# Performance work log

Measured on AMD Instinct MI355X. Metric: run time of the kernel, lower is better.

Reference implementation:

```python
import jax, jax.numpy as jnp
from jax import lax
import numpy as np

B, T, D = 16, 4096, 512          # batch, encoder length, d_model
C, FW = 10, 100                  # aconv_chans, aconv_filts (kernel width 2*FW+1)
SHARP = 2.0                      # sharpening_factor


def setup_inputs() -> dict:
    key = jax.random.key(0)
    ks = jax.random.split(key, 11)
    s = 1.0 / np.sqrt(D)
    sc = 1.0 / np.sqrt(2 * FW + 1)
    return {
        "value": jax.random.normal(ks[0], (B, T, D), jnp.float32),
        "query": jax.random.normal(ks[1], (B, D), jnp.float32),
        "input_lengths": jax.random.randint(ks[2], (B,), T // 2, T + 1),
        "att_prev": jax.random.uniform(ks[3], (B, T), jnp.float32),
        # learned parameters (torch Linear stores W as [out,in]; y = x @ W.T + b)
        "W_enc": jax.random.uniform(ks[4], (D, D), jnp.float32, -s, s),
        "b_enc": jax.random.uniform(ks[5], (D,), jnp.float32, -s, s),
        "W_dec": jax.random.uniform(ks[6], (D, D), jnp.float32, -s, s),
        "W_att": jax.random.uniform(ks[7], (D, C), jnp.float32, -s, s),
        "W_conv": jax.random.uniform(ks[8], (C, 1, 2 * FW + 1), jnp.float32, -sc, sc),
        "w_g": jax.random.uniform(ks[9], (1, D), jnp.float32, -s, s),
        "b_g": jax.random.uniform(ks[10], (1,), jnp.float32, -s, s),
    }


def reference(value, query, input_lengths, att_prev,
              W_enc, b_enc, W_dec, W_att, W_conv, w_g, b_g):
    # pre_compute_enc_h = mlp_enc(enc_h): [B,T,D]
    pre_enc = jnp.einsum('btd,ed->bte', value, W_enc) + b_enc
    # dec_z_tiled = mlp_dec(dec_z): [B,1,D]
    dec_tiled = (query @ W_dec.T)[:, None, :]
    # loc_conv: 1D conv over T, in_ch=1 -> out_ch=C, same padding -> [B,C,T]
    conv = lax.conv_general_dilated(att_prev[:, None, :], W_conv,
                                    window_strides=(1,), padding=[(FW, FW)],
                                    dimension_numbers=('NCH', 'OIH', 'NCH'))
    # mlp_att on transposed conv: [B,T,C] @ W_att.T -> [B,T,D]
    att_conv = jnp.einsum('bct,dc->btd', conv, W_att)
    # e = gvec(tanh(sum)): [B,T]
    e = jnp.einsum('btd,d->bt', jnp.tanh(att_conv + pre_enc + dec_tiled), w_g[0]) + b_g[0]
    # pad mask: positions >= length are masked to -inf (use large finite neg)
    pad_mask = jnp.arange(T)[None, :] >= input_lengths[:, None]
    e = jnp.where(pad_mask, -1e30, e)
    att_weights = jax.nn.softmax(SHARP * e, axis=1)            # [B,T]
    context = jnp.einsum('btd,bt->bd', value, att_weights)     # [B,D]
    return context, att_weights
```

## Files before the change

kernel.cpp:

```cpp
#include <hip/hip_runtime.h>
#include <hip/hip_bf16.h>

constexpr int kB  = 16;
constexpr int kT  = 4096;
constexpr int kD  = 512;
constexpr int kC  = 10;
constexpr int kFW = 100;
constexpr int kKW = 2 * kFW + 1;
constexpr int kKP = 544;
constexpr int kCW = 32;

typedef __attribute__((ext_vector_type(8))) short short8_t;
typedef __attribute__((ext_vector_type(4))) float float4_t;

__device__ __forceinline__ float tanh_fast(float x) {
  float ax = fabsf(x);
  float z  = __expf(-2.0f * ax);
  float r  = (1.0f - z) / (1.0f + z);
  return copysignf(r, x);
}

__device__ __forceinline__ short f2bf(float x) {
  unsigned u = __float_as_uint(x);
  u += 0x7fffu + ((u >> 16) & 1u);
  return (short)(u >> 16);
}

__device__ __forceinline__ unsigned pk2(float lo, float hi) {
  __hip_bfloat162 h = __float22bfloat162_rn(make_float2(lo, hi));
  union { __hip_bfloat162 h2; unsigned u; } cv; cv.h2 = h; return cv.u;
}

__device__ __forceinline__ void glds16(const void* g, void* l) {
  __builtin_amdgcn_global_load_lds(
      (const __attribute__((address_space(1))) void*)g,
      (__attribute__((address_space(3))) void*)l, 16, 0, 0);
}

__global__ void dec_bias_kernel(const float* __restrict__ query,
                                const float* __restrict__ W_dec,
                                const float* __restrict__ b_enc,
                                float* __restrict__ bias) {
  int gw   = (blockIdx.x * blockDim.x + threadIdx.x) >> 6;
  int lane = threadIdx.x & 63;
  int b = gw >> 9;
  int d = gw & (kD - 1);
  const float* q = query + (size_t)b * kD;
  const float* w = W_dec + (size_t)d * kD;
  float s = 0.f;
#pragma unroll
  for (int k0 = 0; k0 < kD; k0 += 256) {
    float4 qa = *(const float4*)(q + k0 + lane * 4);
    float4 wa = *(const float4*)(w + k0 + lane * 4);
    s += qa.x * wa.x + qa.y * wa.y + qa.z * wa.z + qa.w * wa.w;
  }
#pragma unroll
  for (int off = 32; off > 0; off >>= 1) s += __shfl_down(s, off, 64);
  if (lane == 0) bias[gw] = b_enc[d] + s;
}

__global__ void pack_w_kernel(const float* __restrict__ W_enc,
                              const float* __restrict__ W_att,
                              short* __restrict__ Wbf) {
  int d = blockIdx.x;
  for (int c = threadIdx.x; c < kKP; c += 256) {
    float v = 0.f;
    if (c < kD)            v = W_enc[(size_t)d * kD + c];
    else if (c < kD + kC)  v = W_att[(size_t)d * kC + (c - kD)];
    Wbf[(size_t)d * kKP + c] = f2bf(v);
  }
}

__global__ void conv_kernel(const float* __restrict__ att_prev,
                            const float* __restrict__ W_conv,
                            short* __restrict__ convbf) {
  __shared__ float ap[256 + 2 * kFW];
  __shared__ float wc[kC * kKW];
  int b   = blockIdx.y;
  int t0  = blockIdx.x * 256;
  int tid = threadIdx.x;
  for (int i = tid; i < kC * kKW; i += 256) wc[i] = W_conv[i];
  for (int i = tid; i < 256 + 2 * kFW; i += 256) {
    int p = t0 - kFW + i;
    ap[i] = (p >= 0 && p < kT) ? att_prev[(size_t)b * kT + p] : 0.f;
  }
  __syncthreads();
  float acc[kC];
#pragma unroll
  for (int c = 0; c < kC; ++c) acc[c] = 0.f;
  for (int j = 0; j < kKW; ++j) {
    float a = ap[tid + j];
#pragma unroll
    for (int c = 0; c < kC; ++c) acc[c] += a * wc[c * kKW + j];
  }
  unsigned ow[16];
#pragma unroll
  for (int i = 0; i < 5; ++i) ow[i] = pk2(acc[2 * i], acc[2 * i + 1]);
#pragma unroll
  for (int i = 5; i < 16; ++i) ow[i] = 0u;
  uint4* out = (uint4*)(convbf + ((size_t)b * kT + t0 + tid) * kCW);
  out[0] = make_uint4(ow[0], ow[1], ow[2], ow[3]);
  out[1] = make_uint4(ow[4], ow[5], ow[6], ow[7]);
  out[2] = make_uint4(ow[8], ow[9], ow[10], ow[11]);
  out[3] = make_uint4(ow[12], ow[13], ow[14], ow[15]);
}

constexpr int BM = 128, BN = 128, BK = 32;

__global__ __launch_bounds__(256) void e_kernel(
    const float* __restrict__ value, const short* __restrict__ convbf,
    const short* __restrict__ Wbf, const float* __restrict__ bias,
    const float* __restrict__ w_g, const int* __restrict__ lens,
    float* __restrict__ e_part) {
  __shared__ short As[BM * BK];
  __shared__ short Bs[BN * BK];

  int tid = threadIdx.x;
  int L    = blockIdx.x;
  int xcd  = L & 7;
  int slot = L >> 3;
  int bn   = slot & 3;
  int mt   = xcd * 64 + (slot >> 2);
  int b  = mt >> 5;
  int t0 = (mt & 31) * BM;
  if (t0 >= lens[b]) return;
  int n0 = bn * BN;

  int w    = tid >> 6;
  int lane = tid & 63;
  int nl   = lane & 15;
  int quad = lane >> 4;
  int wm = w >> 1, wn = w & 1;

  int srow = tid >> 1, skh = tid & 1;
  int ga = (srow >> 1) & 3;
  const float* aptr = value + ((size_t)(b * kT + t0) + srow) * kD + skh * 16;
  short* aw0 = &As[((srow << 2) + ((skh * 2)     ^ ga)) * 8];
  short* aw1 = &As[((srow << 2) + ((skh * 2 + 1) ^ ga)) * 8];

  int kps = (lane & 3) ^ ((lane >> 3) & 3);
  const short* bsrc0 = Wbf + (size_t)(n0 + w * 32 + (lane >> 2)) * kKP + kps * 8;
  const short* bsrc1 = bsrc0 + (size_t)16 * kKP;
  short* bdst0 = &Bs[(w * 32) * BK];
  short* bdst1 = &Bs[(w * 32 + 16) * BK];

  const short* csrc0 = convbf + ((size_t)(b * kT + t0) + w * 32 + (lane >> 2)) * kCW + kps * 8;
  const short* csrc1 = csrc0 + (size_t)16 * kCW;

  int swz = quad ^ ((nl >> 1) & 3);
  const short8_t* ard = (const short8_t*)&As[(((wm * 64 + nl) << 2) + swz) * 8];
  const short8_t* brd = (const short8_t*)&Bs[(((wn * 64 + nl) << 2) + swz) * 8];

  float4_t acc[4][4] = {};

  float4 pf0 = *(const float4*)(aptr);
  float4 pf1 = *(const float4*)(aptr + 4);
  float4 pf2 = *(const float4*)(aptr + 8);
  float4 pf3 = *(const float4*)(aptr + 12);

  for (int kk = 0; kk < 17; ++kk) {
    __syncthreads();
    glds16(bsrc0 + kk * BK, bdst0);
    glds16(bsrc1 + kk * BK, bdst1);
    if (kk < 16) {
      union { short8_t s8; unsigned u[4]; } c0, c1;
      c0.u[0] = pk2(pf0.x, pf0.y); c0.u[1] = pk2(pf0.z, pf0.w);
      c0.u[2] = pk2(pf1.x, pf1.y); c0.u[3] = pk2(pf1.z, pf1.w);
      c1.u[0] = pk2(pf2.x, pf2.y); c1.u[1] = pk2(pf2.z, pf2.w);
      c1.u[2] = pk2(pf3.x, pf3.y); c1.u[3] = pk2(pf3.z, pf3.w);
      *(short8_t*)aw0 = c0.s8;
      *(short8_t*)aw1 = c1.s8;
    } else {
      glds16(csrc0, (void*)&As[(w * 32) * BK]);
      glds16(csrc1, (void*)&As[(w * 32 + 16) * BK]);
    }
    __syncthreads();
    if (kk < 15) {
      const float* np = aptr + (kk + 1) * BK;
      pf0 = *(const float4*)(np);
      pf1 = *(const float4*)(np + 4);
      pf2 = *(const float4*)(np + 8);
      pf3 = *(const float4*)(np + 12);
    }
    short8_t a_frag[4], b_frag[4];
#pragma unroll
    for (int i = 0; i < 4; ++i) a_frag[i] = ard[i * 64];
#pragma unroll
    for (int j = 0; j < 4; ++j) b_frag[j] = brd[j * 64];
#pragma unroll
    for (int i = 0; i < 4; ++i)
#pragma unroll
      for (int j = 0; j < 4; ++j)
        acc[i][j] = __builtin_amdgcn_mfma_f32_16x16x32_bf16(
            a_frag[i], b_frag[j], acc[i][j], 0, 0, 0);
  }

  float bias_r[4], wg_r[4];
#pragma unroll
  for (int j = 0; j < 4; ++j) {
    int d = n0 + wn * 64 + j * 16 + nl;
    bias_r[j] = bias[b * kD + d];
    wg_r[j]   = w_g[d];
  }
  int p = wn * 4 + bn;
  float* ep = e_part + ((size_t)p * kB + b) * kT + t0 + wm * 64;
#pragma unroll
  for (int i = 0; i < 4; ++i) {
#pragma unroll
    for (int r = 0; r < 4; ++r) {
      float s = 0.f;
#pragma unroll
      for (int j = 0; j < 4; ++j)
        s += wg_r[j] * tanh_fast(acc[i][j][r] + bias_r[j]);
      s += __shfl_xor(s, 1, 64);
      s += __shfl_xor(s, 2, 64);
      s += __shfl_xor(s, 4, 64);
      s += __shfl_xor(s, 8, 64);
      if (nl == 0) ep[i * 16 + quad * 4 + r] = s;
    }
  }
}

__global__ void softmax_kernel(const float* __restrict__ e_part,
                               const int* __restrict__ lens,
                               float* __restrict__ att) {
  __shared__ float eb[kT];
  __shared__ float sred[256];
  int b = blockIdx.x, tid = threadIdx.x;
  int len = lens[b];
  const float* ep = e_part + (size_t)b * kT;
  float m = -3.0e38f;
  for (int t = tid; t < len; t += 256) {
    float s = 0.f;
#pragma unroll
    for (int p = 0; p < 8; ++p) s += ep[(size_t)p * kB * kT + t];
    eb[t] = s;
    m = fmaxf(m, s);
  }
  sred[tid] = m; __syncthreads();
  for (int s = 128; s > 0; s >>= 1) {
    if (tid < s) sred[tid] = fmaxf(sred[tid], sred[tid + s]);
    __syncthreads();
  }
  m = sred[0]; __syncthreads();
  float sum = 0.f;
  for (int t = tid; t < len; t += 256) sum += __expf(2.0f * (eb[t] - m));
  sred[tid] = sum; __syncthreads();
  for (int s = 128; s > 0; s >>= 1) {
    if (tid < s) sred[tid] += sred[tid + s];
    __syncthreads();
  }
  float inv = 1.0f / sred[0];
  for (int t = tid; t < kT; t += 256)
    att[(size_t)b * kT + t] = (t < len) ? __expf(2.0f * (eb[t] - m)) * inv : 0.0f;
}

__global__ void context_kernel(const float* __restrict__ value,
                               const float* __restrict__ att,
                               const int* __restrict__ lens,
                               float* __restrict__ ctx) {
  int b = blockIdx.y;
  int len = lens[b];
  int t0 = blockIdx.x * 128;
  if (t0 >= len) return;
  int tid = threadIdx.x;
  int d4 = (tid & 127) * 4;
  int th = tid >> 7;
  int tb = t0 + th * 64;
  int tmax = min(64, len - tb);
  const float* ap = att + (size_t)b * kT + tb;
  const float* vp = value + ((size_t)(b * kT) + tb) * kD + d4;
  float4 a = {0.f, 0.f, 0.f, 0.f};
#pragma unroll 4
  for (int t = 0; t < tmax; ++t) {
    float wt = ap[t];
    float4 v = *(const float4*)(vp + (size_t)t * kD);
    a.x += wt * v.x; a.y += wt * v.y; a.z += wt * v.z; a.w += wt * v.w;
  }
  if (tmax > 0) {
    atomicAdd(&ctx[b * kD + d4],     a.x);
    atomicAdd(&ctx[b * kD + d4 + 1], a.y);
    atomicAdd(&ctx[b * kD + d4 + 2], a.z);
    atomicAdd(&ctx[b * kD + d4 + 3], a.w);
  }
}

extern "C" void kernel_launch(void* const* d_in, const int* in_sizes, int n_in,
                              void* d_out, int out_size, void* d_ws, size_t ws_size,
                              hipStream_t stream) {
  const float* value    = (const float*)d_in[0];
  const float* query    = (const float*)d_in[1];
  const int*   lens     = (const int*)  d_in[2];
  const float* att_prev = (const float*)d_in[3];
  const float* W_enc    = (const float*)d_in[4];
  const float* b_enc    = (const float*)d_in[5];
  const float* W_dec    = (const float*)d_in[6];
  const float* W_att    = (const float*)d_in[7];
  const float* W_conv   = (const float*)d_in[8];
  const float* w_g      = (const float*)d_in[9];

  float* ws     = (float*)d_ws;
  float* e_part = ws;
  short* convbf = (short*)(ws + (size_t)8 * kB * kT);
  float* bias   = (float*)(convbf + (size_t)kB * kT * kCW);
  short* Wbf    = (short*)(bias + (size_t)kB * kD);
  float* ctx = (float*)d_out;
  float* att = ctx + (size_t)kB * kD;

  hipMemsetAsync(ctx, 0, (size_t)kB * kD * sizeof(float), stream);

  dec_bias_kernel<<<kB * kD / 4, 256, 0, stream>>>(query, W_dec, b_enc, bias);
  pack_w_kernel<<<kD, 256, 0, stream>>>(W_enc, W_att, Wbf);
  conv_kernel<<<dim3(kT / 256, kB), 256, 0, stream>>>(att_prev, W_conv, convbf);
  e_kernel<<<2048, 256, 0, stream>>>(value, convbf, Wbf, bias, w_g, lens, e_part);
  softmax_kernel<<<kB, 256, 0, stream>>>(e_part, lens, att);
  context_kernel<<<dim3(kT / 128, kB), 256, 0, stream>>>(value, att, lens, ctx);
}
```

Measured before the change: 348.8 us.

## Pre-convert value to packed bf16 buffer shared by GEMM and context kernels

After: 325.5 us. 1.07x faster.

```diff
diff --git a/kernel.cpp b/kernel.cpp
--- a/kernel.cpp
+++ b/kernel.cpp
@@ -8,7 +8,6 @@
 constexpr int kFW = 100;
 constexpr int kKW = 2 * kFW + 1;
 constexpr int kKP = 544;
-constexpr int kCW = 32;
 
 typedef __attribute__((ext_vector_type(8))) short short8_t;
 typedef __attribute__((ext_vector_type(4))) float float4_t;
@@ -29,6 +28,10 @@
 __device__ __forceinline__ unsigned pk2(float lo, float hi) {
   __hip_bfloat162 h = __float22bfloat162_rn(make_float2(lo, hi));
   union { __hip_bfloat162 h2; unsigned u; } cv; cv.h2 = h; return cv.u;
+}
+
+__device__ __forceinline__ float bf2f(short s) {
+  return __uint_as_float(((unsigned)(unsigned short)s) << 16);
 }
 
 __device__ __forceinline__ void glds16(const void* g, void* l) {
@@ -71,9 +74,31 @@
   }
 }
 
+__global__ void convert_kernel(const float* __restrict__ value,
+                               const int* __restrict__ lens,
+                               short* __restrict__ Abf) {
+  int b  = blockIdx.y;
+  int t0 = blockIdx.x * 64;
+  if (t0 >= lens[b]) return;
+  int tid = threadIdx.x;
+  const float* src = value + ((size_t)b * kT + t0) * kD;
+  short* dst = Abf + ((size_t)b * kT + t0) * kKP;
+#pragma unroll
+  for (int i = 0; i < 16; ++i) {
+    int c = tid + i * 256;
+    int row = c >> 6, col = (c & 63) * 8;
+    float4 f0 = *(const float4*)(src + (size_t)row * kD + col);
+    float4 f1 = *(const float4*)(src + (size_t)row * kD + col + 4);
+    uint4 o;
+    o.x = pk2(f0.x, f0.y); o.y = pk2(f0.z, f0.w);
+    o.z = pk2(f1.x, f1.y); o.w = pk2(f1.z, f1.w);
+    *(uint4*)(dst + (size_t)row * kKP + col) = o;
+  }
+}
+
 __global__ void conv_kernel(const float* __restrict__ att_prev,
                             const float* __restrict__ W_conv,
-                            short* __restrict__ convbf) {
+                            short* __restrict__ Abf) {
   __shared__ float ap[256 + 2 * kFW];
   __shared__ float wc[kC * kKW];
   int b   = blockIdx.y;
@@ -98,7 +123,7 @@
   for (int i = 0; i < 5; ++i) ow[i] = pk2(acc[2 * i], acc[2 * i + 1]);
 #pragma unroll
   for (int i = 5; i < 16; ++i) ow[i] = 0u;
-  uint4* out = (uint4*)(convbf + ((size_t)b * kT + t0 + tid) * kCW);
+  uint4* out = (uint4*)(Abf + ((size_t)b * kT + t0 + tid) * kKP + kD);
   out[0] = make_uint4(ow[0], ow[1], ow[2], ow[3]);
   out[1] = make_uint4(ow[4], ow[5], ow[6], ow[7]);
   out[2] = make_uint4(ow[8], ow[9], ow[10], ow[11]);
@@ -108,10 +133,9 @@
 constexpr int BM = 128, BN = 128, BK = 32;
 
 __global__ __launch_bounds__(256) void e_kernel(
-    const float* __restrict__ value, const short* __restrict__ convbf,
-    const short* __restrict__ Wbf, const float* __restrict__ bias,
-    const float* __restrict__ w_g, const int* __restrict__ lens,
-    float* __restrict__ e_part) {
+    const short* __restrict__ Abf, const short* __restrict__ Wbf,
+    const float* __restrict__ bias, const float* __restrict__ w_g,
+    const int* __restrict__ lens, float* __restrict__ e_part) {
   __shared__ short As[BM * BK];
   __shared__ short Bs[BN * BK];
 
@@ -132,56 +156,30 @@
   int quad = lane >> 4;
   int wm = w >> 1, wn = w & 1;
 
-  int srow = tid >> 1, skh = tid & 1;
-  int ga = (srow >> 1) & 3;
-  const float* aptr = value + ((size_t)(b * kT + t0) + srow) * kD + skh * 16;
-  short* aw0 = &As[((srow << 2) + ((skh * 2)     ^ ga)) * 8];
-  short* aw1 = &As[((srow << 2) + ((skh * 2 + 1) ^ ga)) * 8];
-
   int kps = (lane & 3) ^ ((lane >> 3) & 3);
+  const short* asrc0 = Abf + ((size_t)(b * kT + t0) + w * 32 + (lane >> 2)) * kKP + kps * 8;
+  const short* asrc1 = asrc0 + (size_t)16 * kKP;
+  short* adst0 = &As[(w * 32) * BK];
+  short* adst1 = &As[(w * 32 + 16) * BK];
   const short* bsrc0 = Wbf + (size_t)(n0 + w * 32 + (lane >> 2)) * kKP + kps * 8;
   const short* bsrc1 = bsrc0 + (size_t)16 * kKP;
   short* bdst0 = &Bs[(w * 32) * BK];
   short* bdst1 = &Bs[(w * 32 + 16) * BK];
 
-  const short* csrc0 = convbf + ((size_t)(b * kT + t0) + w * 32 + (lane >> 2)) * kCW + kps * 8;
-  const short* csrc1 = csrc0 + (size_t)16 * kCW;
-
   int swz = quad ^ ((nl >> 1) & 3);
   const short8_t* ard = (const short8_t*)&As[(((wm * 64 + nl) << 2) + swz) * 8];
   const short8_t* brd = (const short8_t*)&Bs[(((wn * 64 + nl) << 2) + swz) * 8];
 
   float4_t acc[4][4] = {};
 
-  float4 pf0 = *(const float4*)(aptr);
-  float4 pf1 = *(const float4*)(aptr + 4);
-  float4 pf2 = *(const float4*)(aptr + 8);
-  float4 pf3 = *(const float4*)(aptr + 12);
-
   for (int kk = 0; kk < 17; ++kk) {
+    int ko = kk * BK;
     __syncthreads();
-    glds16(bsrc0 + kk * BK, bdst0);
-    glds16(bsrc1 + kk * BK, bdst1);
-    if (kk < 16) {
-      union { short8_t s8; unsigned u[4]; } c0, c1;
-      c0.u[0] = pk2(pf0.x, pf0.y); c0.u[1] = pk2(pf0.z, pf0.w);
-      c0.u[2] = pk2(pf1.x, pf1.y); c0.u[3] = pk2(pf1.z, pf1.w);
-      c1.u[0] = pk2(pf2.x, pf2.y); c1.u[1] = pk2(pf2.z, pf2.w);
-      c1.u[2] = pk2(pf3.x, pf3.y); c1.u[3] = pk2(pf3.z, pf3.w);
-      *(short8_t*)aw0 = c0.s8;
-      *(short8_t*)aw1 = c1.s8;
-    } else {
-      glds16(csrc0, (void*)&As[(w * 32) * BK]);
-      glds16(csrc1, (void*)&As[(w * 32 + 16) * BK]);
-    }
+    glds16(asrc0 + ko, adst0);
+    glds16(asrc1 + ko, adst1);
+    glds16(bsrc0 + ko, bdst0);
+    glds16(bsrc1 + ko, bdst1);
     __syncthreads();
-    if (kk < 15) {
-      const float* np = aptr + (kk + 1) * BK;
-      pf0 = *(const float4*)(np);
-      pf1 = *(const float4*)(np + 4);
-      pf2 = *(const float4*)(np + 8);
-      pf3 = *(const float4*)(np + 12);
-    }
     short8_t a_frag[4], b_frag[4];
 #pragma unroll
     for (int i = 0; i < 4; ++i) a_frag[i] = ard[i * 64];
@@ -255,33 +253,34 @@
     att[(size_t)b * kT + t] = (t < len) ? __expf(2.0f * (eb[t] - m)) * inv : 0.0f;
 }
 
-__global__ void context_kernel(const float* __restrict__ value,
+__global__ void context_kernel(const short* __restrict__ Abf,
                                const float* __restrict__ att,
                                const int* __restrict__ lens,
                                float* __restrict__ ctx) {
+  __shared__ float red[4][kD];
   int b = blockIdx.y;
   int len = lens[b];
   int t0 = blockIdx.x * 128;
   if (t0 >= len) return;
-  int tid = threadIdx.x;
-  int d4 = (tid & 127) * 4;
-  int th = tid >> 7;
-  int tb = t0 + th * 64;
-  int tmax = min(64, len - tb);
+  int w = threadIdx.x >> 6, lane = threadIdx.x & 63;
+  int tb = t0 + w * 32;
+  int tmax = min(32, len - tb);
+  float a[8] = {0.f, 0.f, 0.f, 0.f, 0.f, 0.f, 0.f, 0.f};
+  const short* vp = Abf + ((size_t)b * kT + tb) * kKP + lane * 8;
   const float* ap = att + (size_t)b * kT + tb;
-  const float* vp = value + ((size_t)(b * kT) + tb) * kD + d4;
-  float4 a = {0.f, 0.f, 0.f, 0.f};
-#pragma unroll 4
   for (int t = 0; t < tmax; ++t) {
     float wt = ap[t];
-    float4 v = *(const float4*)(vp + (size_t)t * kD);
-    a.x += wt * v.x; a.y += wt * v.y; a.z += wt * v.z; a.w += wt * v.w;
-  }
-  if (tmax > 0) {
-    atomicAdd(&ctx[b * kD + d4],     a.x);
-    atomicAdd(&ctx[b * kD + d4 + 1], a.y);
-    atomicAdd(&ctx[b * kD + d4 + 2], a.z);
-    atomicAdd(&ctx[b * kD + d4 + 3], a.w);
+    short8_t v = *(const short8_t*)(vp + (size_t)t * kKP);
+#pragma unroll
+    for (int i = 0; i < 8; ++i) a[i] += wt * bf2f(v[i]);
+  }
+#pragma unroll
+  for (int i = 0; i < 8; ++i) red[w][lane * 8 + i] = a[i];
+  __syncthreads();
+  int tid = threadIdx.x;
+  for (int col = tid; col < kD; col += 256) {
+    float s = red[0][col] + red[1][col] + red[2][col] + red[3][col];
+    atomicAdd(&ctx[b * kD + col], s);
   }
 }
 
@@ -301,9 +300,9 @@
 
   float* ws     = (float*)d_ws;
   float* e_part = ws;
-  short* convbf = (short*)(ws + (size_t)8 * kB * kT);
-  float* bias   = (float*)(convbf + (size_t)kB * kT * kCW);
+  float* bias   = e_part + (size_t)8 * kB * kT;
   short* Wbf    = (short*)(bias + (size_t)kB * kD);
+  short* Abf    = Wbf + (size_t)kD * kKP;
   float* ctx = (float*)d_out;
   float* att = ctx + (size_t)kB * kD;
 
@@ -311,8 +310,9 @@
 
   dec_bias_kernel<<<kB * kD / 4, 256, 0, stream>>>(query, W_dec, b_enc, bias);
   pack_w_kernel<<<kD, 256, 0, stream>>>(W_enc, W_att, Wbf);
-  conv_kernel<<<dim3(kT / 256, kB), 256, 0, stream>>>(att_prev, W_conv, convbf);
-  e_kernel<<<2048, 256, 0, stream>>>(value, convbf, Wbf, bias, w_g, lens, e_part);
+  convert_kernel<<<dim3(kT / 64, kB), 256, 0, stream>>>(value, lens, Abf);
+  conv_kernel<<<dim3(kT / 256, kB), 256, 0, stream>>>(att_prev, W_conv, Abf);
+  e_kernel<<<2048, 256, 0, stream>>>(Abf, Wbf, bias, w_g, lens, e_part);
   softmax_kernel<<<kB, 256, 0, stream>>>(e_part, lens, att);
-  context_kernel<<<dim3(kT / 128, kB), 256, 0, stream>>>(value, att, lens, ctx);
-}
+  context_kernel<<<dim3(kT / 128, kB), 256, 0, stream>>>(Abf, att, lens, ctx);
+}
```
